# Kernel tuning notes

Hardware: AMD Instinct MI355X
Metric: run time of the kernel (lower is better)

The kernel has to match this reference:

```python
import jax, jax.numpy as jnp
import numpy as np

B, C, D, J = 8, 2048, 128, 128

def setup_inputs() -> dict:
    key = jax.random.key(0)
    ks = jax.random.split(key, 24)
    s = 0.02
    inp = {
        "operation_features": jax.random.normal(ks[0], (B, C, D), jnp.float32),
        "relations": jax.random.randint(ks[1], (B, C - 2, 2), 0, C, jnp.int64),
        "begins_idx": jax.random.randint(ks[2], (B, J), 0, C, jnp.int64),
        "ends_idx": jax.random.randint(ks[3], (B, J), 0, C, jnp.int64),
        "same_type_mask": (jax.random.uniform(ks[4], (B, C, C)) > 0.5).astype(jnp.float32),
        # BeginEndEncoder
        "W_begin": jax.random.normal(ks[5], (D, D), jnp.float32) * s,
        "b_begin": jnp.zeros((D,), jnp.float32),
        "W_end": jax.random.normal(ks[6], (D, D), jnp.float32) * s,
        "b_end": jnp.zeros((D,), jnp.float32),
        # OperationTimeRelationEncoder.mix: Linear(3D -> D)
        "W_mix3": jax.random.normal(ks[7], (3 * D, D), jnp.float32) * s,
        "b_mix3": jnp.zeros((D,), jnp.float32),
        # SelfAttention (hidden_dim = D)
        "W_qkv": jax.random.normal(ks[8], (D, 3 * D), jnp.float32) * s,
        "b_qkv": jnp.zeros((3 * D,), jnp.float32),
        "w_score": jax.random.normal(ks[9], (2 * D,), jnp.float32) * s,
        "b_score": jnp.zeros((), jnp.float32),
        "W_out": jax.random.normal(ks[10], (D, D), jnp.float32) * s,
        "b_out": jnp.zeros((D,), jnp.float32),
        # block mix: Linear(2D -> D)
        "W_mix2": jax.random.normal(ks[11], (2 * D, D), jnp.float32) * s,
        "b_mix2": jnp.zeros((D,), jnp.float32),
    }
    return inp

def _gather_ops(ops, idx):
    # ops: [B,C,D], idx: [B,M] -> [B,M,D]  (torch.gather along dim 1 with expanded index)
    Bb, _, Dd = ops.shape
    M = idx.shape[1]
    return jnp.take_along_axis(ops, jnp.broadcast_to(idx[:, :, None], (Bb, M, Dd)), axis=1)

def reference(operation_features, relations, begins_idx, ends_idx, same_type_mask,
              W_begin, b_begin, W_end, b_end, W_mix3, b_mix3,
              W_qkv, b_qkv, w_score, b_score, W_out, b_out, W_mix2, b_mix2):
    ops = operation_features
    Dd = ops.shape[-1]
    # --- OperationTimeRelationEncoder ---
    pred = _gather_ops(ops, relations[..., 0])      # [B,C-2,D]
    succ = _gather_ops(ops, relations[..., 1])      # [B,C-2,D]
    concated = jnp.concatenate([ops[:, :-2, :], pred, succ], axis=-1)  # [B,C-2,3D]
    mixed = concated @ W_mix3 + b_mix3              # [B,C-2,D]
    begin_f = _gather_ops(ops, begins_idx) @ W_begin + b_begin  # [B,J,D]
    end_f = _gather_ops(ops, ends_idx) @ W_end + b_end
    begin = jnp.mean(begin_f, axis=1)               # [B,D]
    end = jnp.mean(end_f, axis=1)
    seq = jnp.concatenate([mixed, begin[:, None, :], end[:, None, :]], axis=1)  # [B,C,D]
    # --- SelfAttention (GAT-style additive score, decomposed to avoid CxCx2h blowup) ---
    qkv = ops @ W_qkv + b_qkv                       # [B,C,3D]
    q, k, v = jnp.split(qkv, 3, axis=-1)
    sq = q @ w_score[:Dd]                           # [B,C]  q_i . w_q
    sk = k @ w_score[Dd:]                           # [B,C]  k_j . w_k
    scores = jax.nn.leaky_relu(sq[:, :, None] + sk[:, None, :] + b_score)  # [B,C,C]
    attn = jax.nn.softmax(scores * same_type_mask, axis=-1)                # multiplicative mask, as in torch
    weighted = jnp.einsum('bij,bjd->bid', attn, v)  # [B,C,D]
    same_type = weighted @ W_out + b_out            # [B,C,D]
    # --- final mix ---
    return jnp.concatenate([seq, same_type], axis=-1) @ W_mix2 + b_mix2  # [B,C,D]
```

## Files before the change

### kernel.cpp

```cpp
#include <hip/hip_runtime.h>
#include <cstddef>

typedef __bf16 bf16;
typedef __bf16 bf16x4 __attribute__((ext_vector_type(4)));
typedef __bf16 bf16x8 __attribute__((ext_vector_type(8)));
typedef float  f32x4  __attribute__((ext_vector_type(4)));

#define MFMA16(a, b, c) __builtin_amdgcn_mfma_f32_16x16x32_bf16((a), (b), (c), 0, 0, 0)

#define BB 8
#define CC 2048
#define DD 128
#define JJN 128

#define WS_PK    ((size_t)0)
#define WS_OPS16 ((size_t)8388608)
#define WS_SQF   ((size_t)12582912)
#define WS_SKF   ((size_t)12648448)
#define WS_G1T   ((size_t)12713984)
#define WS_G2T   ((size_t)12746752)
#define WS_G3T   ((size_t)12779520)
#define WS_WCT   ((size_t)12812288)
#define WS_GBT   ((size_t)12845056)
#define WS_GET   ((size_t)12877824)
#define WS_UQK   ((size_t)12910592)
#define WS_BBM   ((size_t)12911104)
#define WS_BBB   ((size_t)12911616)
#define WS_BBE   ((size_t)12912128)
#define WS_SC    ((size_t)12912640)
#define WS_WCN   ((size_t)12913152)
#define WS_GBN   ((size_t)12945920)
#define WS_GEN   ((size_t)12978688)
#define WS_MB    ((size_t)13011456)
#define WS_MEANV ((size_t)17205760)

__global__ __launch_bounds__(256) void k_prepcast(
    const float* __restrict__ ops, bf16* __restrict__ ops16,
    const float* __restrict__ mask, const int* __restrict__ begins,
    const int* __restrict__ ends,
    const float* __restrict__ Wmix3, const float* __restrict__ Wmix2,
    const float* __restrict__ Wout,  const float* __restrict__ Wbegin,
    const float* __restrict__ Wend,  const float* __restrict__ Wqkv,
    const float* __restrict__ bqkv,  const float* __restrict__ wscore,
    const float* __restrict__ bscore,const float* __restrict__ bmix3,
    const float* __restrict__ bout,  const float* __restrict__ bmix2,
    const float* __restrict__ bbegin,const float* __restrict__ bend,
    bf16* __restrict__ G1T, bf16* __restrict__ G2T, bf16* __restrict__ G3T,
    bf16* __restrict__ WCT, bf16* __restrict__ GBT, bf16* __restrict__ GET,
    bf16* __restrict__ WCN, bf16* __restrict__ GBN, bf16* __restrict__ GEN,
    bf16* __restrict__ uqk, float* __restrict__ BBM, float* __restrict__ BBB,
    float* __restrict__ BBE, float* __restrict__ sc,
    unsigned char* __restrict__ MBITS, float* __restrict__ MEANV)
{
    __shared__ bf16  LshT[128 * 132];
    __shared__ float Rsh[128 * 8];
    int wg = blockIdx.x;
    int t  = threadIdx.x;

    if (wg == 0) {
        for (int half = 0; half < 2; ++half) {
            #pragma unroll
            for (int pass = 0; pass < 16; ++pass) {
                int idx = pass * 256 + t;
                int d   = idx >> 5;
                int e0  = (idx & 31) * 4;
                f32x4 v = *(const f32x4*)(Wqkv + d*384 + half*128 + e0);
                #pragma unroll
                for (int jj = 0; jj < 4; ++jj)
                    LshT[(e0 + jj)*132 + d] = (bf16)v[jj];
            }
            if (t < 32) {
                f32x4 wv = *(const f32x4*)(wscore + half*128 + t*4);
                #pragma unroll
                for (int jj = 0; jj < 4; ++jj) Rsh[t*4 + jj] = wv[jj];
            }
            __syncthreads();
            if (t < 128) {
                float s = 0.f;
                for (int e = 0; e < 128; ++e)
                    s += (float)LshT[e*132 + t] * Rsh[e];
                uqk[half*128 + t] = (bf16)s;
            }
            __syncthreads();
        }
        float bm = 0.f, bb_ = 0.f, be_ = 0.f, bon = 0.f;
        for (int half = 0; half < 2; ++half) {
            #pragma unroll
            for (int pass = 0; pass < 16; ++pass) {
                int idx = pass * 256 + t;
                int f   = idx >> 5;
                int e0  = (idx & 31) * 4;
                f32x4 v = *(const f32x4*)(Wmix2 + (size_t)(half*128 + f)*128 + e0);
                #pragma unroll
                for (int jj = 0; jj < 4; ++jj)
                    LshT[f*132 + e0 + jj] = (bf16)v[jj];
            }
            if (t < 32) {
                if (half == 0) {
                    f32x4 v0 = *(const f32x4*)(bmix3  + t*4);
                    f32x4 v1 = *(const f32x4*)(bbegin + t*4);
                    f32x4 v2 = *(const f32x4*)(bend   + t*4);
                    #pragma unroll
                    for (int jj = 0; jj < 4; ++jj) {
                        Rsh[t*4 + jj]       = v0[jj];
                        Rsh[128 + t*4 + jj] = v1[jj];
                        Rsh[256 + t*4 + jj] = v2[jj];
                    }
                } else {
                    f32x4 v3 = *(const f32x4*)(bout + t*4);
                    #pragma unroll
                    for (int jj = 0; jj < 4; ++jj) Rsh[t*4 + jj] = v3[jj];
                }
            }
            __syncthreads();
            if (t < 128) {
                if (half == 0) {
                    for (int f = 0; f < 128; ++f) {
                        float wv = (float)LshT[f*132 + t];
                        bm  += Rsh[f]       * wv;
                        bb_ += Rsh[128 + f] * wv;
                        be_ += Rsh[256 + f] * wv;
                    }
                } else {
                    for (int f = 0; f < 128; ++f)
                        bon += Rsh[f] * (float)LshT[f*132 + t];
                }
            }
            __syncthreads();
        }
        if (t < 128) {
            float bm2 = bmix2[t];
            BBM[t] = bm  + bon + bm2;
            BBB[t] = bb_ + bon + bm2;
            BBE[t] = be_ + bon + bm2;
        }
        if (t >= 128) {
            int e2 = t - 128;
            Rsh[512 + e2] = bqkv[e2]       * wscore[e2];
            Rsh[640 + e2] = bqkv[128 + e2] * wscore[128 + e2];
        }
        __syncthreads();
        if (t == 0) {
            float cq = 0.f, ck = 0.f;
            for (int e2 = 0; e2 < 128; ++e2) {
                cq += Rsh[512 + e2];
                ck += Rsh[640 + e2];
            }
            sc[0] = cq + bscore[0];
            sc[1] = ck;
        }
        return;
    }
    if (wg <= 16) {
        int task = wg - 1;
        int b2 = task >> 1, which = task & 1;
        const int* idxp = which ? (ends + b2 * JJN) : (begins + b2 * JJN);
        int* ish = (int*)Rsh;
        if (t < JJN) ish[t] = idxp[t];
        __syncthreads();
        int d = t & 127, half = t >> 7;
        const float* opsb = ops + (size_t)b2 * CC * DD;
        float s = 0.f;
        #pragma unroll 8
        for (int j = 0; j < 64; ++j) {
            int r = ish[half * 64 + j];
            s += opsb[(size_t)r * DD + d];
        }
        float* fsh = Rsh + 256;
        fsh[half * 128 + d] = s;
        __syncthreads();
        if (t < 128)
            MEANV[task * 128 + t] = (fsh[t] + fsh[128 + t]) * (1.0f / (float)JJN);
        return;
    }
    if (wg <= 2064) {
        int p = wg - 17;
        size_t base = (size_t)p * 16384;
        const float* mp = mask + base;
        unsigned char* ob = MBITS + (base >> 3);
        #pragma unroll
        for (int k = 0; k < 8; ++k) {
            size_t fo = (size_t)k * 2048 + (size_t)t * 8;
            f32x4 a = __builtin_nontemporal_load((const f32x4*)(mp + fo));
            f32x4 c = __builtin_nontemporal_load((const f32x4*)(mp + fo + 4));
            unsigned byte = 0;
            #pragma unroll
            for (int e = 0; e < 4; ++e) {
                byte |= (a[e] != 0.f ? 1u : 0u) << e;
                byte |= (c[e] != 0.f ? 1u : 0u) << (4 + e);
            }
            ob[k * 256 + t] = (unsigned char)byte;
        }
        return;
    }
    if (wg <= 2160) {
        int id  = wg - 2065;
        int mat = id >> 4, sub = id & 15;
        const float* L; const float* R; bf16* O; bf16* O2;
        switch (mat) {
            case 0: L = Wmix3;           R = Wmix2;           O = G1T; O2 = nullptr; break;
            case 1: L = Wmix3 + 128*128; R = Wmix2;           O = G2T; O2 = nullptr; break;
            case 2: L = Wmix3 + 256*128; R = Wmix2;           O = G3T; O2 = nullptr; break;
            case 3: L = Wout;            R = Wmix2 + 128*128; O = WCT; O2 = WCN; break;
            case 4: L = Wbegin;          R = Wmix2;           O = GBT; O2 = GBN; break;
            default:L = Wend;            R = Wmix2;           O = GET; O2 = GEN; break;
        }
        int e0 = sub * 8;
        #pragma unroll
        for (int pass = 0; pass < 16; ++pass) {
            int idx = pass * 256 + t;
            int d   = idx >> 5;
            int f0  = (idx & 31) * 4;
            f32x4 v = *(const f32x4*)(L + d * 128 + f0);
            #pragma unroll
            for (int jj = 0; jj < 4; ++jj)
                LshT[(f0 + jj) * 132 + d] = (bf16)v[jj];
        }
        #pragma unroll
        for (int pass = 0; pass < 4; ++pass) {
            int idx = pass * 256 + t;
            int f   = idx >> 3;
            int ee  = idx & 7;
            Rsh[f * 8 + ee] = R[f * 128 + e0 + ee];
        }
        __syncthreads();
        int ee = t >> 5;
        int e  = e0 + ee;
        int d0 = (t & 31) * 4;
        float s[4] = {0.f, 0.f, 0.f, 0.f};
        for (int f = 0; f < 128; ++f) {
            bf16x4 lv = *(const bf16x4*)&LshT[f * 132 + d0];
            float rv = Rsh[f * 8 + ee];
            #pragma unroll
            for (int dd = 0; dd < 4; ++dd)
                s[dd] += (float)lv[dd] * rv;
        }
        #pragma unroll
        for (int dd = 0; dd < 4; ++dd) {
            O[e * 128 + d0 + dd] = (bf16)s[dd];
            if (O2) O2[(d0 + dd) * 128 + e] = (bf16)s[dd];
        }
        return;
    }
    size_t i = (size_t)(wg - 2161) * 256 + t;
    f32x4 a = *(const f32x4*)(ops + i * 8);
    f32x4 b = *(const f32x4*)(ops + i * 8 + 4);
    bf16x8 o;
    #pragma unroll
    for (int e = 0; e < 4; ++e) { o[e] = (bf16)a[e]; o[4 + e] = (bf16)b[e]; }
    *(bf16x8*)(ops16 + i * 8) = o;
}

__global__ __launch_bounds__(256) void k_v(
    const bf16* __restrict__ ops16, const float* __restrict__ Wqkv,
    const float* __restrict__ bqkv, const bf16* __restrict__ uqk,
    const float* __restrict__ sc,
    bf16* __restrict__ PK, float* __restrict__ sqf, float* __restrict__ skf)
{
    __shared__ bf16 A[144 * 136];
    int b  = blockIdx.x & 7;
    int jt = (blockIdx.x >> 3) * 64;
    int t  = threadIdx.x;
    #pragma unroll
    for (int pass = 0; pass < 16; ++pass) {
        int idx = pass * 256 + t;
        int d   = idx >> 5;
        int n0  = (idx & 31) * 4;
        f32x4 v = *(const f32x4*)(Wqkv + d*384 + 256 + n0);
        #pragma unroll
        for (int jj = 0; jj < 4; ++jj)
            A[(n0 + jj)*136 + d] = (bf16)v[jj];
    }
    {
        int row = t >> 7, col = t & 127;
        A[(128 + row)*136 + col] = uqk[row*128 + col];
    }
    for (int idx = t; idx < 14*136; idx += 256)
        A[130*136 + idx] = (bf16)0.f;
    __syncthreads();

    int lane = t & 63, w = t >> 6;
    int m = lane & 15, q = lane >> 4;
    f32x4 acc[9];
    #pragma unroll
    for (int rb = 0; rb < 9; ++rb) acc[rb] = {0.f, 0.f, 0.f, 0.f};

    const bf16* opsb = ops16 + (size_t)b * CC * DD;
    int j = jt + w*16 + m;
    #pragma unroll
    for (int kc = 0; kc < 4; ++kc) {
        bf16x8 bfr = *(const bf16x8*)(opsb + (size_t)j*DD + kc*32 + q*8);
        #pragma unroll
        for (int rb = 0; rb < 9; ++rb) {
            bf16x8 afr = *(const bf16x8*)&A[(rb*16 + m)*136 + kc*32 + q*8];
            acc[rb] = MFMA16(afr, bfr, acc[rb]);
        }
    }
    float cqb = sc[0], ckv = sc[1];
    if (q == 0) {
        sqf[b*CC + j] = acc[8][0] + cqb;
        skf[b*CC + j] = acc[8][1] + ckv;
    }
    __syncthreads();
    bf16* pack = A;
    {
        int jcl = w >> 1;
        int qv  = (w & 1) * 2 + (m >> 3);
        int ev  = m & 7;
        #pragma unroll
        for (int rb = 0; rb < 8; ++rb) {
            #pragma unroll
            for (int r = 0; r < 4; ++r) {
                float v = acc[rb][r] + bqkv[256 + rb*16 + q*4 + r];
                pack[jcl*4096 + rb*512 + qv*128 + (q*4+r)*8 + ev] = (bf16)v;
            }
        }
    }
    __syncthreads();
    bf16* pkb = PK + (size_t)b * DD * CC + (size_t)jt * 128;
    #pragma unroll
    for (int pass = 0; pass < 4; ++pass) {
        int lidx = pass * 256 + t;
        *(uint4*)(pkb + (size_t)lidx * 8) = *(const uint4*)&pack[lidx * 8];
    }
}

__device__ __forceinline__ void load_vb(const bf16* __restrict__ pkb, int jc,
                                        int q, int m, bf16x8 vb[8])
{
    #pragma unroll
    for (int nb = 0; nb < 8; ++nb)
        vb[nb] = *(const bf16x8*)(pkb + ((size_t)(((jc*8 + nb)*4 + q)*16 + m)) * 8);
}

__global__ __launch_bounds__(512, 4) void k_attepi(
    const unsigned char* __restrict__ MBITS, const bf16* __restrict__ PK,
    const float* __restrict__ sqf, const float* __restrict__ skf,
    const bf16* __restrict__ ops16, const int* __restrict__ relations,
    const bf16* __restrict__ G1T, const bf16* __restrict__ G2T,
    const bf16* __restrict__ G3T, const bf16* __restrict__ WCT,
    const bf16* __restrict__ GBN, const bf16* __restrict__ GEN,
    const bf16* __restrict__ WCN,
    const float* __restrict__ BBM, const float* __restrict__ BBB,
    const float* __restrict__ BBE, const float* __restrict__ MEANV,
    float* __restrict__ out)
{
    __shared__ __align__(16) char smem[52224];
    int t    = threadIdx.x;
    int lane = t & 63, w = t >> 6;
    int b    = blockIdx.x & 7;
    int i0   = (blockIdx.x >> 3) << 5;
    int m = lane & 15, q = lane >> 4;

    unsigned char* Lb  = (unsigned char*)smem;
    float*         skw = (float*)(smem + 8704 + w * 1024);

    {
        int row = t >> 4, seg = t & 15;
        *(uint4*)(Lb + row * 272 + seg * 16) = *(const uint4*)(MBITS
            + ((size_t)(b * CC + i0 + row)) * 256 + seg * 16);
    }
    *(f32x4*)(skw + lane * 4) = *(const f32x4*)(skf + b * CC + w * 256 + lane * 4);

    float sq0 = sqf[b * CC + i0 + m];
    float sq1 = sqf[b * CC + i0 + 16 + m];
    const bf16* pkb = PK + (size_t)b * DD * CC;
    int jc0 = w * 8;

    f32x4 acc0[8], acc1[8];
    #pragma unroll
    for (int nb = 0; nb < 8; ++nb) {
        acc0[nb] = {0.f, 0.f, 0.f, 0.f};
        acc1[nb] = {0.f, 0.f, 0.f, 0.f};
    }
    float lsum0 = 0.f, lsum1 = 0.f;
    __syncthreads();

    #pragma unroll
    for (int c = 0; c < 8; ++c) {
        bf16x8 vb[8];
        load_vb(pkb, jc0 + c, q, m, vb);
        int bo = (jc0 + c) * 4 + q;
        unsigned mb0 = Lb[m * 272 + bo];
        unsigned mb1 = Lb[(16 + m) * 272 + bo];
        int jo = c * 32 + q * 8;
        f32x4 s0 = *(const f32x4*)(skw + jo);
        f32x4 s1 = *(const f32x4*)(skw + jo + 4);
        float sks[8] = {s0[0], s0[1], s0[2], s0[3], s1[0], s1[1], s1[2], s1[3]};
        bf16x8 a0, a1;
        #pragma unroll
        for (int e = 0; e < 8; ++e) {
            float sk = sks[e];
            float t0 = sq0 + sk;
            float l0 = fmaxf(t0, 0.01f * t0);
            float p0 = __expf(l0 * (float)((mb0 >> e) & 1u));
            lsum0 += p0;
            a0[e] = (bf16)p0;
            float t1 = sq1 + sk;
            float l1 = fmaxf(t1, 0.01f * t1);
            float p1 = __expf(l1 * (float)((mb1 >> e) & 1u));
            lsum1 += p1;
            a1[e] = (bf16)p1;
        }
        #pragma unroll
        for (int nb = 0; nb < 8; ++nb) {
            acc0[nb] = MFMA16(a0, vb[nb], acc0[nb]);
            acc1[nb] = MFMA16(a1, vb[nb], acc1[nb]);
        }
    }
    __syncthreads();

    float* Osh  = (float*)(smem + 8704);
    float* Lsh  = (float*)(smem + 42496);
    bf16*  Obuf = (bf16*)(smem + 43520);
    #pragma unroll
    for (int tile = 0; tile < 2; ++tile) {
        float ls = tile ? lsum1 : lsum0;
        ls += __shfl_xor(ls, 16, 64);
        ls += __shfl_xor(ls, 32, 64);
        const f32x4* acc = tile ? acc1 : acc0;
        if (w < 4) {
            if (q == 0) Lsh[w*16 + m] = ls;
            #pragma unroll
            for (int nb = 0; nb < 8; ++nb)
                #pragma unroll
                for (int r = 0; r < 4; ++r)
                    Osh[(w*16 + q*4 + r)*132 + nb*16 + m] = acc[nb][r];
        }
        __syncthreads();
        if (w >= 4) {
            if (q == 0) Lsh[(w-4)*16 + m] += ls;
            #pragma unroll
            for (int nb = 0; nb < 8; ++nb)
                #pragma unroll
                for (int r = 0; r < 4; ++r)
                    Osh[((w-4)*16 + q*4 + r)*132 + nb*16 + m] += acc[nb][r];
        }
        __syncthreads();
        if (t < 256) {
            int r   = t >> 4;
            int c0e = (t & 15) * 8;
            float l = Lsh[r] + Lsh[16 + r] + Lsh[32 + r] + Lsh[48 + r];
            float inv = 1.0f / l;
            bf16x8 o;
            #pragma unroll
            for (int e = 0; e < 8; ++e) {
                float s = Osh[r*132 + c0e + e] + Osh[(16 + r)*132 + c0e + e]
                        + Osh[(32 + r)*132 + c0e + e] + Osh[(48 + r)*132 + c0e + e];
                o[e] = (bf16)(s * inv);
            }
            *(bf16x8*)&Obuf[(tile * 16 + r) * 136 + c0e] = o;
        }
        __syncthreads();
    }

    bf16* Abuf = (bf16*)smem;
    bf16* Bbuf = (bf16*)(smem + 8704);

    f32x4 eacc[2];
    eacc[0] = {0.f, 0.f, 0.f, 0.f};
    eacc[1] = {0.f, 0.f, 0.f, 0.f};

    const bf16* Bsrc[4] = {G1T, G2T, G3T, WCT};
    int arow = t >> 4, ao = (t & 15) * 8;
    int brow = t >> 2, bo2 = (t & 3) * 32;
    int c = i0 + arow;

    for (int term = 0; term < 4; ++term) {
        if (term < 3) {
            const bf16* src;
            if (term == 0) src = ops16 + ((size_t)(b * CC + c)) * DD;
            else {
                int ridx = relations[((size_t)b * (CC - 2) + min(c, CC - 3)) * 2 + (term - 1)];
                src = ops16 + ((size_t)(b * CC) + ridx) * DD;
            }
            *(uint4*)&Abuf[arow * 136 + ao] = *(const uint4*)(src + ao);
        }
        #pragma unroll
        for (int ii = 0; ii < 4; ++ii)
            *(uint4*)&Bbuf[brow * 136 + bo2 + ii*8] =
                *(const uint4*)(Bsrc[term] + brow * 128 + bo2 + ii*8);
        __syncthreads();

        const bf16* Asrc = (term == 3) ? Obuf : Abuf;
        #pragma unroll
        for (int kc = 0; kc < 4; ++kc) {
            bf16x8 bfr = *(const bf16x8*)&Bbuf[(w*16 + m)*136 + kc*32 + q*8];
            #pragma unroll
            for (int rb = 0; rb < 2; ++rb) {
                bf16x8 afr = *(const bf16x8*)&Asrc[(rb*16 + m)*136 + kc*32 + q*8];
                eacc[rb] = MFMA16(afr, bfr, eacc[rb]);
            }
        }
        __syncthreads();
    }
    {
        int col = w*16 + m;
        float bias = BBM[col];
        #pragma unroll
        for (int rb = 0; rb < 2; ++rb) {
            #pragma unroll
            for (int r = 0; r < 4; ++r) {
                int cg = i0 + rb*16 + q*4 + r;
                if (cg < CC - 2)
                    out[((size_t)(b * CC) + cg) * DD + col] = eacc[rb][r] + bias;
            }
        }
    }

    if (i0 == CC - 32) {
        __syncthreads();
        float* mv2 = (float*)smem;
        if (t < 256)
            mv2[(t >> 7) * 128 + (t & 127)] =
                MEANV[((size_t)b * 2 + (t >> 7)) * 128 + (t & 127)];
        __syncthreads();
        if (t < 256) {
            int grp = t >> 7, tl = t & 127;
            int which = grp;
            const bf16* G    = which ? GEN : GBN;
            const float* Bv  = which ? BBE : BBB;
            const bf16* orow = Obuf + (30 + which) * 136;
            float a = Bv[tl];
            const float* mv = mv2 + grp * 128;
            for (int d = 0; d < 128; ++d) {
                a += mv[d] * (float)G[d * 128 + tl];
                a += (float)orow[d] * (float)WCN[d * 128 + tl];
            }
            out[((size_t)b * CC + (CC - 2 + which)) * DD + tl] = a;
        }
    }
}

extern "C" void kernel_launch(void* const* d_in, const int* in_sizes, int n_in,
                              void* d_out, int out_size, void* d_ws, size_t ws_size,
                              hipStream_t stream)
{
    const float* ops      = (const float*)d_in[0];
    const int*  relations = (const int*)d_in[1];
    const int*  begins    = (const int*)d_in[2];
    const int*  ends      = (const int*)d_in[3];
    const float* mask     = (const float*)d_in[4];
    const float* Wbegin   = (const float*)d_in[5];
    const float* bbegin   = (const float*)d_in[6];
    const float* Wend     = (const float*)d_in[7];
    const float* bend     = (const float*)d_in[8];
    const float* Wmix3    = (const float*)d_in[9];
    const float* bmix3    = (const float*)d_in[10];
    const float* Wqkv     = (const float*)d_in[11];
    const float* bqkv     = (const float*)d_in[12];
    const float* wscore   = (const float*)d_in[13];
    const float* bscore   = (const float*)d_in[14];
    const float* Wout     = (const float*)d_in[15];
    const float* bout     = (const float*)d_in[16];
    const float* Wmix2    = (const float*)d_in[17];
    const float* bmix2    = (const float*)d_in[18];
    float* outp = (float*)d_out;

    char* ws = (char*)d_ws;
    bf16*  PK    = (bf16*)(ws + WS_PK);
    bf16*  OPS16 = (bf16*)(ws + WS_OPS16);
    float* sqf   = (float*)(ws + WS_SQF);
    float* skf   = (float*)(ws + WS_SKF);
    bf16*  G1T   = (bf16*)(ws + WS_G1T);
    bf16*  G2T   = (bf16*)(ws + WS_G2T);
    bf16*  G3T   = (bf16*)(ws + WS_G3T);
    bf16*  WCT   = (bf16*)(ws + WS_WCT);
    bf16*  GBT   = (bf16*)(ws + WS_GBT);
    bf16*  GET   = (bf16*)(ws + WS_GET);
    bf16*  WCN   = (bf16*)(ws + WS_WCN);
    bf16*  GBN   = (bf16*)(ws + WS_GBN);
    bf16*  GEN   = (bf16*)(ws + WS_GEN);
    bf16*  UQK   = (bf16*)(ws + WS_UQK);
    float* BBM   = (float*)(ws + WS_BBM);
    float* BBB   = (float*)(ws + WS_BBB);
    float* BBE   = (float*)(ws + WS_BBE);
    float* SC    = (float*)(ws + WS_SC);
    unsigned char* MBITS = (unsigned char*)(ws + WS_MB);
    float* MEANV = (float*)(ws + WS_MEANV);

    k_prepcast<<<dim3(3185), dim3(256), 0, stream>>>(
        ops, OPS16, mask, begins, ends,
        Wmix3, Wmix2, Wout, Wbegin, Wend, Wqkv, bqkv, wscore, bscore,
        bmix3, bout, bmix2, bbegin, bend,
        G1T, G2T, G3T, WCT, GBT, GET, WCN, GBN, GEN,
        UQK, BBM, BBB, BBE, SC, MBITS, MEANV);

    k_v<<<dim3(256), dim3(256), 0, stream>>>(
        OPS16, Wqkv, bqkv, UQK, SC, PK, sqf, skf);

    k_attepi<<<dim3(512), dim3(512), 0, stream>>>(
        MBITS, PK, sqf, skf, OPS16, relations,
        G1T, G2T, G3T, WCT, GBN, GEN, WCN, BBM, BBB, BBE, MEANV, outp);
}
```

Baseline: 316.4 us.

## Move mask bit-packing into k_v and re-split attention warps across rows and key ranges

The mask-to-bitmask conversion blocks move from the prep kernel into the k_v launch as extra blocks, so the large mask read can overlap with the value/projection work. In the attention kernel, each warp now handles one 16-row tile over a quarter of the keys, instead of two row tiles over an eighth. This halves the accumulator registers per warp and leaves a two-plane reduction instead of four-way reductions repeated per tile. The launch bound drops from 4 to 2 blocks per CU, which allows more registers but may reduce occupancy.

```diff
diff --git a/kernel.cpp b/kernel.cpp
--- a/kernel.cpp
+++ b/kernel.cpp
@@ -36,8 +36,7 @@
 
 __global__ __launch_bounds__(256) void k_prepcast(
     const float* __restrict__ ops, bf16* __restrict__ ops16,
-    const float* __restrict__ mask, const int* __restrict__ begins,
-    const int* __restrict__ ends,
+    const int* __restrict__ begins, const int* __restrict__ ends,
     const float* __restrict__ Wmix3, const float* __restrict__ Wmix2,
     const float* __restrict__ Wout,  const float* __restrict__ Wbegin,
     const float* __restrict__ Wend,  const float* __restrict__ Wqkv,
@@ -49,8 +48,7 @@
     bf16* __restrict__ WCT, bf16* __restrict__ GBT, bf16* __restrict__ GET,
     bf16* __restrict__ WCN, bf16* __restrict__ GBN, bf16* __restrict__ GEN,
     bf16* __restrict__ uqk, float* __restrict__ BBM, float* __restrict__ BBB,
-    float* __restrict__ BBE, float* __restrict__ sc,
-    unsigned char* __restrict__ MBITS, float* __restrict__ MEANV)
+    float* __restrict__ BBE, float* __restrict__ sc, float* __restrict__ MEANV)
 {
     __shared__ bf16  LshT[128 * 132];
     __shared__ float Rsh[128 * 8];
@@ -173,28 +171,8 @@
             MEANV[task * 128 + t] = (fsh[t] + fsh[128 + t]) * (1.0f / (float)JJN);
         return;
     }
-    if (wg <= 2064) {
-        int p = wg - 17;
-        size_t base = (size_t)p * 16384;
-        const float* mp = mask + base;
-        unsigned char* ob = MBITS + (base >> 3);
-        #pragma unroll
-        for (int k = 0; k < 8; ++k) {
-            size_t fo = (size_t)k * 2048 + (size_t)t * 8;
-            f32x4 a = __builtin_nontemporal_load((const f32x4*)(mp + fo));
-            f32x4 c = __builtin_nontemporal_load((const f32x4*)(mp + fo + 4));
-            unsigned byte = 0;
-            #pragma unroll
-            for (int e = 0; e < 4; ++e) {
-                byte |= (a[e] != 0.f ? 1u : 0u) << e;
-                byte |= (c[e] != 0.f ? 1u : 0u) << (4 + e);
-            }
-            ob[k * 256 + t] = (unsigned char)byte;
-        }
-        return;
-    }
-    if (wg <= 2160) {
-        int id  = wg - 2065;
+    if (wg <= 112) {
+        int id  = wg - 17;
         int mat = id >> 4, sub = id & 15;
         const float* L; const float* R; bf16* O; bf16* O2;
         switch (mat) {
@@ -242,7 +220,7 @@
         }
         return;
     }
-    size_t i = (size_t)(wg - 2161) * 256 + t;
+    size_t i = (size_t)(wg - 113) * 256 + t;
     f32x4 a = *(const f32x4*)(ops + i * 8);
     f32x4 b = *(const f32x4*)(ops + i * 8 + 4);
     bf16x8 o;
@@ -254,13 +232,34 @@
 __global__ __launch_bounds__(256) void k_v(
     const bf16* __restrict__ ops16, const float* __restrict__ Wqkv,
     const float* __restrict__ bqkv, const bf16* __restrict__ uqk,
-    const float* __restrict__ sc,
-    bf16* __restrict__ PK, float* __restrict__ sqf, float* __restrict__ skf)
+    const float* __restrict__ sc,   const float* __restrict__ mask,
+    bf16* __restrict__ PK, float* __restrict__ sqf, float* __restrict__ skf,
+    unsigned char* __restrict__ MBITS)
 {
     __shared__ bf16 A[144 * 136];
+    int t = threadIdx.x;
+    if (blockIdx.x >= 256) {
+        int p = blockIdx.x - 256;
+        size_t base = (size_t)p * 16384;
+        const float* mp = mask + base;
+        unsigned char* ob = MBITS + (base >> 3);
+        #pragma unroll
+        for (int k = 0; k < 8; ++k) {
+            size_t fo = (size_t)k * 2048 + (size_t)t * 8;
+            f32x4 a = __builtin_nontemporal_load((const f32x4*)(mp + fo));
+            f32x4 c = __builtin_nontemporal_load((const f32x4*)(mp + fo + 4));
+            unsigned byte = 0;
+            #pragma unroll
+            for (int e = 0; e < 4; ++e) {
+                byte |= (a[e] != 0.f ? 1u : 0u) << e;
+                byte |= (c[e] != 0.f ? 1u : 0u) << (4 + e);
+            }
+            ob[k * 256 + t] = (unsigned char)byte;
+        }
+        return;
+    }
     int b  = blockIdx.x & 7;
     int jt = (blockIdx.x >> 3) * 64;
-    int t  = threadIdx.x;
     #pragma unroll
     for (int pass = 0; pass < 16; ++pass) {
         int idx = pass * 256 + t;
@@ -333,7 +332,7 @@
         vb[nb] = *(const bf16x8*)(pkb + ((size_t)(((jc*8 + nb)*4 + q)*16 + m)) * 8);
 }
 
-__global__ __launch_bounds__(512, 4) void k_attepi(
+__global__ __launch_bounds__(512, 2) void k_attepi(
     const unsigned char* __restrict__ MBITS, const bf16* __restrict__ PK,
     const float* __restrict__ sqf, const float* __restrict__ skf,
     const bf16* __restrict__ ops16, const int* __restrict__ relations,
@@ -351,106 +350,93 @@
     int b    = blockIdx.x & 7;
     int i0   = (blockIdx.x >> 3) << 5;
     int m = lane & 15, q = lane >> 4;
+    int tl = w & 1;
+    int jg = w >> 1;
 
     unsigned char* Lb  = (unsigned char*)smem;
-    float*         skw = (float*)(smem + 8704 + w * 1024);
+    float*         skw = (float*)(smem + 8704);
 
     {
         int row = t >> 4, seg = t & 15;
         *(uint4*)(Lb + row * 272 + seg * 16) = *(const uint4*)(MBITS
             + ((size_t)(b * CC + i0 + row)) * 256 + seg * 16);
     }
-    *(f32x4*)(skw + lane * 4) = *(const f32x4*)(skf + b * CC + w * 256 + lane * 4);
-
-    float sq0 = sqf[b * CC + i0 + m];
-    float sq1 = sqf[b * CC + i0 + 16 + m];
+    *(f32x4*)(skw + t * 4) = *(const f32x4*)(skf + b * CC + t * 4);
+
+    float sq = sqf[b * CC + i0 + tl * 16 + m];
     const bf16* pkb = PK + (size_t)b * DD * CC;
-    int jc0 = w * 8;
-
-    f32x4 acc0[8], acc1[8];
-    #pragma unroll
-    for (int nb = 0; nb < 8; ++nb) {
-        acc0[nb] = {0.f, 0.f, 0.f, 0.f};
-        acc1[nb] = {0.f, 0.f, 0.f, 0.f};
-    }
-    float lsum0 = 0.f, lsum1 = 0.f;
+    const float* skg = skw + jg * 512;
+
+    f32x4 acc[8];
+    #pragma unroll
+    for (int nb = 0; nb < 8; ++nb) acc[nb] = {0.f, 0.f, 0.f, 0.f};
+    float lsum = 0.f;
     __syncthreads();
 
     #pragma unroll
-    for (int c = 0; c < 8; ++c) {
+    for (int c = 0; c < 16; ++c) {
+        int jc = jg * 16 + c;
         bf16x8 vb[8];
-        load_vb(pkb, jc0 + c, q, m, vb);
-        int bo = (jc0 + c) * 4 + q;
-        unsigned mb0 = Lb[m * 272 + bo];
-        unsigned mb1 = Lb[(16 + m) * 272 + bo];
+        load_vb(pkb, jc, q, m, vb);
+        unsigned mb = Lb[(tl * 16 + m) * 272 + jc * 4 + q];
         int jo = c * 32 + q * 8;
-        f32x4 s0 = *(const f32x4*)(skw + jo);
-        f32x4 s1 = *(const f32x4*)(skw + jo + 4);
+        f32x4 s0 = *(const f32x4*)(skg + jo);
+        f32x4 s1 = *(const f32x4*)(skg + jo + 4);
         float sks[8] = {s0[0], s0[1], s0[2], s0[3], s1[0], s1[1], s1[2], s1[3]};
-        bf16x8 a0, a1;
+        bf16x8 a;
         #pragma unroll
         for (int e = 0; e < 8; ++e) {
-            float sk = sks[e];
-            float t0 = sq0 + sk;
-            float l0 = fmaxf(t0, 0.01f * t0);
-            float p0 = __expf(l0 * (float)((mb0 >> e) & 1u));
-            lsum0 += p0;
-            a0[e] = (bf16)p0;
-            float t1 = sq1 + sk;
-            float l1 = fmaxf(t1, 0.01f * t1);
-            float p1 = __expf(l1 * (float)((mb1 >> e) & 1u));
-            lsum1 += p1;
-            a1[e] = (bf16)p1;
-        }
-        #pragma unroll
-        for (int nb = 0; nb < 8; ++nb) {
-            acc0[nb] = MFMA16(a0, vb[nb], acc0[nb]);
-            acc1[nb] = MFMA16(a1, vb[nb], acc1[nb]);
-        }
-    }
+            float tv = sq + sks[e];
+            float lr = fmaxf(tv, 0.01f * tv);
+            float p  = __expf(lr * (float)((mb >> e) & 1u));
+            lsum += p;
+            a[e] = (bf16)p;
+        }
+        #pragma unroll
+        for (int nb = 0; nb < 8; ++nb)
+            acc[nb] = MFMA16(a, vb[nb], acc[nb]);
+    }
+
+    lsum += __shfl_xor(lsum, 16, 64);
+    lsum += __shfl_xor(lsum, 32, 64);
+
     __syncthreads();
 
     float* Osh  = (float*)(smem + 8704);
     float* Lsh  = (float*)(smem + 42496);
     bf16*  Obuf = (bf16*)(smem + 43520);
-    #pragma unroll
-    for (int tile = 0; tile < 2; ++tile) {
-        float ls = tile ? lsum1 : lsum0;
-        ls += __shfl_xor(ls, 16, 64);
-        ls += __shfl_xor(ls, 32, 64);
-        const f32x4* acc = tile ? acc1 : acc0;
-        if (w < 4) {
-            if (q == 0) Lsh[w*16 + m] = ls;
+    {
+        int plane = jg & 1;
+        int orow  = plane * 32 + tl * 16;
+        if (jg < 2) {
+            if (q == 0) Lsh[plane * 32 + tl * 16 + m] = lsum;
             #pragma unroll
             for (int nb = 0; nb < 8; ++nb)
                 #pragma unroll
                 for (int r = 0; r < 4; ++r)
-                    Osh[(w*16 + q*4 + r)*132 + nb*16 + m] = acc[nb][r];
-        }
-        __syncthreads();
-        if (w >= 4) {
-            if (q == 0) Lsh[(w-4)*16 + m] += ls;
+                    Osh[(orow + q * 4 + r) * 132 + nb * 16 + m] = acc[nb][r];
+        }
+        __syncthreads();
+        if (jg >= 2) {
+            if (q == 0) Lsh[plane * 32 + tl * 16 + m] += lsum;
             #pragma unroll
             for (int nb = 0; nb < 8; ++nb)
                 #pragma unroll
                 for (int r = 0; r < 4; ++r)
-                    Osh[((w-4)*16 + q*4 + r)*132 + nb*16 + m] += acc[nb][r];
-        }
-        __syncthreads();
-        if (t < 256) {
-            int r   = t >> 4;
-            int c0e = (t & 15) * 8;
-            float l = Lsh[r] + Lsh[16 + r] + Lsh[32 + r] + Lsh[48 + r];
-            float inv = 1.0f / l;
-            bf16x8 o;
-            #pragma unroll
-            for (int e = 0; e < 8; ++e) {
-                float s = Osh[r*132 + c0e + e] + Osh[(16 + r)*132 + c0e + e]
-                        + Osh[(32 + r)*132 + c0e + e] + Osh[(48 + r)*132 + c0e + e];
-                o[e] = (bf16)(s * inv);
-            }
-            *(bf16x8*)&Obuf[(tile * 16 + r) * 136 + c0e] = o;
-        }
+                    Osh[(orow + q * 4 + r) * 132 + nb * 16 + m] += acc[nb][r];
+        }
+        __syncthreads();
+        int r   = t >> 4;
+        int c0e = (t & 15) * 8;
+        float l = Lsh[r] + Lsh[32 + r];
+        float inv = 1.0f / l;
+        bf16x8 o;
+        #pragma unroll
+        for (int e = 0; e < 8; ++e) {
+            float s = Osh[r * 132 + c0e + e] + Osh[(32 + r) * 132 + c0e + e];
+            o[e] = (bf16)(s * inv);
+        }
+        *(bf16x8*)&Obuf[r * 136 + c0e] = o;
         __syncthreads();
     }
 
@@ -516,18 +502,18 @@
                 MEANV[((size_t)b * 2 + (t >> 7)) * 128 + (t & 127)];
         __syncthreads();
         if (t < 256) {
-            int grp = t >> 7, tl = t & 127;
+            int grp = t >> 7, tlx = t & 127;
             int which = grp;
             const bf16* G    = which ? GEN : GBN;
             const float* Bv  = which ? BBE : BBB;
             const bf16* orow = Obuf + (30 + which) * 136;
-            float a = Bv[tl];
+            float a = Bv[tlx];
             const float* mv = mv2 + grp * 128;
             for (int d = 0; d < 128; ++d) {
-                a += mv[d] * (float)G[d * 128 + tl];
-                a += (float)orow[d] * (float)WCN[d * 128 + tl];
-            }
-            out[((size_t)b * CC + (CC - 2 + which)) * DD + tl] = a;
+                a += mv[d] * (float)G[d * 128 + tlx];
+                a += (float)orow[d] * (float)WCN[d * 128 + tlx];
+            }
+            out[((size_t)b * CC + (CC - 2 + which)) * DD + tlx] = a;
         }
     }
 }
@@ -579,15 +565,15 @@
     unsigned char* MBITS = (unsigned char*)(ws + WS_MB);
     float* MEANV = (float*)(ws + WS_MEANV);
 
-    k_prepcast<<<dim3(3185), dim3(256), 0, stream>>>(
-        ops, OPS16, mask, begins, ends,
+    k_prepcast<<<dim3(1137), dim3(256), 0, stream>>>(
+        ops, OPS16, begins, ends,
         Wmix3, Wmix2, Wout, Wbegin, Wend, Wqkv, bqkv, wscore, bscore,
         bmix3, bout, bmix2, bbegin, bend,
         G1T, G2T, G3T, WCT, GBT, GET, WCN, GBN, GEN,
-        UQK, BBM, BBB, BBE, SC, MBITS, MEANV);
-
-    k_v<<<dim3(256), dim3(256), 0, stream>>>(
-        OPS16, Wqkv, bqkv, UQK, SC, PK, sqf, skf);
+        UQK, BBM, BBB, BBE, SC, MEANV);
+
+    k_v<<<dim3(2304), dim3(256), 0, stream>>>(
+        OPS16, Wqkv, bqkv, UQK, SC, mask, PK, sqf, skf, MBITS);
 
     k_attepi<<<dim3(512), dim3(512), 0, stream>>>(
         MBITS, PK, sqf, skf, OPS16, relations,
```

Measured after the change: 279.5 us. 1.13x faster.
